# Performance work log

Measured on AMD Instinct MI355X. Metric: run time of the kernel, lower is better.

The kernel has to match this reference:

```python
import jax, jax.numpy as jnp
import numpy as np

B, S, T, M, H = 16, 128, 1024, 16, 1024
HID = 1024        # attention MLP hidden
WIDTH_EMB = 20    # width embedding dim
N_LING = 2        # len(linguistic_feature_types)


def setup_inputs() -> dict:
    key = jax.random.key(0)
    ks = jax.random.split(key, 12)
    doc_embeddings = jax.random.normal(ks[0], (B, T, H), dtype=jnp.float32)
    start_mappings = jax.random.normal(ks[1], (B, S, T), dtype=jnp.float32)
    end_mappings = jax.random.normal(ks[2], (B, S, T), dtype=jnp.float32)
    continuous_mappings = jax.random.normal(ks[3], (B, S, M, T), dtype=jnp.float32)
    width = jax.random.randint(ks[4], (B, S), 0, M, dtype=jnp.int64)
    linguistic_labels = jax.random.normal(ks[5], (B, S, N_LING), dtype=jnp.float32)
    # attention MLP params (torch Linear layout transposed to x @ W + b)
    W1 = jax.random.normal(ks[6], (H, HID), dtype=jnp.float32) * (1.0 / np.sqrt(H))
    b1 = jax.random.normal(ks[7], (HID,), dtype=jnp.float32) * 0.01
    W2 = jax.random.normal(ks[8], (HID, 1), dtype=jnp.float32) * (1.0 / np.sqrt(HID))
    b2 = jax.random.normal(ks[9], (1,), dtype=jnp.float32) * 0.01
    width_table = jax.random.normal(ks[10], (5, WIDTH_EMB), dtype=jnp.float32)
    return {
        'doc_embeddings': doc_embeddings,
        'start_mappings': start_mappings,
        'end_mappings': end_mappings,
        'continuous_mappings': continuous_mappings,
        'linguistic_labels': linguistic_labels,
        'W1': W1, 'b1': b1, 'W2': W2, 'b2': b2,
        'width_table': width_table,
        'width': width,
    }


def reference(doc_embeddings, start_mappings, end_mappings, continuous_mappings,
              linguistic_labels, W1, b1, W2, b2, width_table, width):
    # one-hot matmul gathers
    start = jnp.einsum('bst,bth->bsh', start_mappings, doc_embeddings)
    end = jnp.einsum('bst,bth->bsh', end_mappings, doc_embeddings)
    cont = jnp.einsum('bsmt,bth->bsmh', continuous_mappings, doc_embeddings)
    b, s, m, h = cont.shape
    vector = jnp.concatenate([start, end], axis=-1).reshape(b * s, 2 * h)
    cont = cont.reshape(b * s, m, h)
    w = width.reshape(b * s)
    ling = linguistic_labels.reshape(b * s, -1)
    # padded masked attention pooling
    masks = (jnp.arange(m)[None, :] < jnp.maximum(w, 1)[:, None]).astype(cont.dtype)
    hdn = jax.nn.relu(jnp.einsum('nmh,hk->nmk', cont, W1) + b1)
    scores = (jnp.einsum('nmk,ko->nmo', hdn, W2) + b2)[..., 0]  # [n, m]
    scores = scores * masks
    scores = jnp.where(scores != 0, scores, jnp.asarray(-9e9, scores.dtype))
    att = jax.nn.softmax(scores, axis=1)
    weighted_sum = jnp.einsum('nm,nmh->nh', att, cont)
    vector = jnp.concatenate([vector, weighted_sum], axis=1)
    # linguistic feature columns (loop over fixed small feature list)
    for fi in range(N_LING):
        vector = jnp.concatenate([vector, ling[:, fi:fi + 1]], axis=1)
    # width embedding (clamp max=4)
    wemb = width_table[jnp.clip(w, 0, 4)]
    vector = jnp.concatenate([vector, wemb], axis=1)
    return vector.reshape(b, s, -1)
```

## Files before the change

### kernel.cpp

```cpp
#include <hip/hip_runtime.h>

typedef unsigned short ushort_t;
typedef unsigned int uint_t;
typedef _Float16 f16;
typedef f16 f16x8 __attribute__((ext_vector_type(8)));
typedef float f32x4 __attribute__((ext_vector_type(4)));

#define B_   16
#define S_   128
#define T_   1024
#define M_   16
#define H_   1024
#define OUTW 3094
#define NSPAN (B_*S_)
#define NROW  (NSPAN*M_)

#define WS_CONT   0
#define WS_DOCT   67108864
#define WS_W1T    100663296
#define WS_SCORES 102760448
#define WS_A16    102891520
#define WS_NEED_A16 178388992ULL

__device__ __forceinline__ float sane(float v) {
  return fminf(fmaxf(v, -60000.f), 60000.f);
}
__device__ __forceinline__ ushort_t f16bits(float f) {
  union { f16 h; ushort_t u; } c; c.h = (f16)f; return c.u;
}
__device__ __forceinline__ void load_lds16(const void* g, void* l) {
  __builtin_amdgcn_global_load_lds(
      (const __attribute__((address_space(1))) uint_t*)g,
      (__attribute__((address_space(3))) uint_t*)l, 16, 0, 0);
}

__device__ __forceinline__ void tconv1024(const float* __restrict__ ip,
                                          ushort_t* __restrict__ op,
                                          uint_t (*tile)[65],
                                          int bx, int by, int tid) {
  const int c0 = bx * 64, r0 = by * 64;
  const int tx = tid & 63, ty = tid >> 6;
#pragma unroll
  for (int p = 0; p < 16; ++p) {
    int r = p * 4 + ty;
    tile[r][tx] = (uint_t)f16bits(ip[(size_t)(r0 + r) * 1024 + c0 + tx]);
  }
  __syncthreads();
  const int rr = (tid & 31) * 2, cc0 = tid >> 5;
  uint_t* op32 = (uint_t*)op;
#pragma unroll
  for (int p = 0; p < 8; ++p) {
    int c = cc0 + p * 8;
    uint_t lo = tile[rr][c] & 0xffffu;
    uint_t hi = tile[rr + 1][c] & 0xffffu;
    op32[((size_t)(c0 + c) * 1024 + r0 + rr) >> 1] = lo | (hi << 16);
  }
}

__global__ __launch_bounds__(256) void prep(const float* __restrict__ doc,
                                            ushort_t* __restrict__ docT,
                                            const float* __restrict__ W1,
                                            ushort_t* __restrict__ W1T,
                                            const float* __restrict__ startm,
                                            const float* __restrict__ endm,
                                            const float* __restrict__ contm,
                                            f16* __restrict__ A16,
                                            float* __restrict__ scores) {
  __shared__ uint_t tile[64][65];
  const int blk = blockIdx.x;
  const int tid = threadIdx.x;
  if (blk < 4096) {
    const int z = blk >> 8, by = (blk >> 4) & 15, bx = blk & 15;
    const size_t mo = (size_t)z * 1024 * 1024;
    tconv1024(doc + mo, docT + mo, tile, bx, by, tid);
  } else if (blk < 4352) {
    const int r2 = blk - 4096;
    tconv1024(W1, W1T, tile, r2 & 15, r2 >> 4, tid);
  } else if (blk < 6400) {
    const int lb = blk - 4352;
    uint_t c = (uint_t)lb * 256u + (uint_t)tid;
#pragma unroll 1
    for (int it = 0; it < 9; ++it) {
      const uint_t b   = c / 294912u;
      const uint_t rem = c - b * 294912u;
      const uint_t r   = rem >> 7;
      const uint_t col = (rem & 127u) << 3;
      const float* src;
      if (r < 128u)      src = startm + ((size_t)b * S_ + r) * T_;
      else if (r < 256u) src = endm + ((size_t)b * S_ + (r - 128u)) * T_;
      else               src = contm + ((size_t)b * S_ * M_ + (r - 256u)) * T_;
      f32x4 lo = *(const f32x4*)(src + col);
      f32x4 hi = *(const f32x4*)(src + col + 4);
      f16x8 h;
#pragma unroll
      for (int k = 0; k < 4; ++k) { h[k] = (f16)lo[k]; h[k + 4] = (f16)hi[k]; }
      *(f16x8*)(A16 + ((size_t)b * 2304 + r) * T_ + col) = h;
      c += 2048u * 256u;
    }
  } else {
    const int idx = (blk - 6400) * 256 + tid;
    scores[idx] = 0.f;
  }
}

__global__ __launch_bounds__(256) void tconv(const float* __restrict__ in,
                                             ushort_t* __restrict__ out,
                                             int R, int C) {
  __shared__ uint_t tile[64][65];
  const int tid = threadIdx.x;
  const size_t mo = (size_t)blockIdx.z * R * C;
  tconv1024(in + mo, out + mo, tile, blockIdx.x, blockIdx.y, tid);
}

__global__ __launch_bounds__(256) void gemm1f(const f16* __restrict__ A16,
                                              const ushort_t* __restrict__ docT,
                                              float* __restrict__ out,
                                              f16* __restrict__ contF) {
  __shared__ f16 As[128 * 32];
  __shared__ ushort_t Bs[128 * 32];
  const int tid = threadIdx.x;
  const uint_t pid = blockIdx.x;
  const int xcd = pid & 7;
  const int s_  = pid >> 3;
  const int ct  = s_ & 7;
  const int pg  = (s_ >> 3) * 8 + xcd;
  const int rt  = pg >> 4;
  const int b   = pg & 15;

  const f16* Ap = A16 + ((size_t)b * 2304 + (size_t)rt * 128) * T_;
  const ushort_t* Bp = docT + (size_t)b * (H_ * T_) + (size_t)ct * 128 * T_;

  const int lane = tid & 63, w = tid >> 6;
  const int wr = w >> 1, wc = w & 1;
  const int quad = lane >> 4, l16 = lane & 15;
  const int srow = lane >> 2;
  const int scol = ((lane & 3) ^ ((lane >> 3) & 3)) * 8;

  f32x4 acc[4][4];
#pragma unroll
  for (int i = 0; i < 4; ++i)
#pragma unroll
    for (int j = 0; j < 4; ++j) acc[i][j] = (f32x4){0.f, 0.f, 0.f, 0.f};

  for (int k0 = 0; k0 < T_; k0 += 32) {
#pragma unroll
    for (int i = 0; i < 2; ++i) {
      const int rb = w * 32 + i * 16;
      load_lds16(Ap + (size_t)(rb + srow) * T_ + k0 + scol, &As[rb * 32]);
    }
#pragma unroll
    for (int i = 0; i < 2; ++i) {
      const int rb = w * 32 + i * 16;
      load_lds16(Bp + (size_t)(rb + srow) * T_ + k0 + scol, &Bs[rb * 32]);
    }
    __syncthreads();
    f16x8 af[4], bfr[4];
#pragma unroll
    for (int i = 0; i < 4; ++i) {
      const int row = wr * 64 + i * 16 + l16;
      const int sw = (row >> 1) & 3;
      af[i] = *(const f16x8*)&As[row * 32 + ((quad ^ sw) * 8)];
    }
#pragma unroll
    for (int j = 0; j < 4; ++j) {
      const int row = wc * 64 + j * 16 + l16;
      const int sw = (row >> 1) & 3;
      bfr[j] = *(const f16x8*)&Bs[row * 32 + ((quad ^ sw) * 8)];
    }
#pragma unroll
    for (int i = 0; i < 4; ++i)
#pragma unroll
      for (int j = 0; j < 4; ++j)
        acc[i][j] = __builtin_amdgcn_mfma_f32_16x16x32_f16(af[i], bfr[j], acc[i][j], 0, 0, 0);
    __syncthreads();
  }

  if (rt < 2) {
    float* op = out + (size_t)b * S_ * OUTW + (size_t)rt * 1024 + (size_t)ct * 128;
#pragma unroll
    for (int i = 0; i < 4; ++i)
#pragma unroll
      for (int j = 0; j < 4; ++j)
#pragma unroll
        for (int r = 0; r < 4; ++r) {
          int row = wr * 64 + i * 16 + quad * 4 + r;
          int col = wc * 64 + j * 16 + l16;
          op[(size_t)row * OUTW + col] = sane(acc[i][j][r]);
        }
  } else {
    f16* cp = contF + ((size_t)b * 2048 + (size_t)(rt - 2) * 128) * H_ + (size_t)ct * 128;
#pragma unroll
    for (int i = 0; i < 4; ++i)
#pragma unroll
      for (int j = 0; j < 4; ++j)
#pragma unroll
        for (int r = 0; r < 4; ++r) {
          int row = wr * 64 + i * 16 + quad * 4 + r;
          int col = wc * 64 + j * 16 + l16;
          cp[(size_t)row * H_ + col] = (f16)sane(acc[i][j][r]);
        }
  }
}

__global__ __launch_bounds__(256) void gemm1(const float* __restrict__ startm,
                                             const float* __restrict__ endm,
                                             const float* __restrict__ contm,
                                             const ushort_t* __restrict__ docT,
                                             float* __restrict__ out,
                                             f16* __restrict__ contF) {
  __shared__ float As[128 * 32];
  __shared__ ushort_t Bs[128 * 32];
  const int tid = threadIdx.x;
  const uint_t pid = blockIdx.x;
  const int xcd = pid & 7;
  const int s_  = pid >> 3;
  const int ct  = s_ & 7;
  const int pg  = (s_ >> 3) * 8 + xcd;
  const int rt  = pg >> 4;
  const int b   = pg & 15;

  const float* Ap;
  if (rt == 0)      Ap = startm + (size_t)b * S_ * T_;
  else if (rt == 1) Ap = endm + (size_t)b * S_ * T_;
  else              Ap = contm + (size_t)b * (S_ * M_ * T_) + (size_t)(rt - 2) * 128 * T_;
  const ushort_t* Bp = docT + (size_t)b * (H_ * T_) + (size_t)ct * 128 * T_;

  const int lane = tid & 63, w = tid >> 6;
  const int wr = w >> 1, wc = w & 1;
  const int quad = lane >> 4, l16 = lane & 15;
  const int arow = lane >> 3;
  const int acol = ((lane & 7) ^ arow) * 4;
  const int brow = lane >> 2;
  const int bcol = ((lane & 3) ^ ((lane >> 3) & 3)) * 8;

  f32x4 acc[4][4];
#pragma unroll
  for (int i = 0; i < 4; ++i)
#pragma unroll
    for (int j = 0; j < 4; ++j) acc[i][j] = (f32x4){0.f, 0.f, 0.f, 0.f};

  for (int k0 = 0; k0 < T_; k0 += 32) {
#pragma unroll
    for (int i = 0; i < 4; ++i) {
      const int rb = w * 32 + i * 8;
      load_lds16(Ap + (size_t)(rb + arow) * T_ + k0 + acol, &As[rb * 32]);
    }
#pragma unroll
    for (int i = 0; i < 2; ++i) {
      const int rb = w * 32 + i * 16;
      load_lds16(Bp + (size_t)(rb + brow) * T_ + k0 + bcol, &Bs[rb * 32]);
    }
    __syncthreads();
    f16x8 af[4], bfr[4];
#pragma unroll
    for (int i = 0; i < 4; ++i) {
      const int row = wr * 64 + i * 16 + l16;
      const int sw = row & 7;
      f32x4 lo = *(const f32x4*)&As[row * 32 + (((quad * 2) ^ sw) * 4)];
      f32x4 hi = *(const f32x4*)&As[row * 32 + (((quad * 2 + 1) ^ sw) * 4)];
      f16x8 h;
#pragma unroll
      for (int k = 0; k < 4; ++k) { h[k] = (f16)lo[k]; h[k + 4] = (f16)hi[k]; }
      af[i] = h;
    }
#pragma unroll
    for (int j = 0; j < 4; ++j) {
      const int row = wc * 64 + j * 16 + l16;
      const int sw = (row >> 1) & 3;
      bfr[j] = *(const f16x8*)&Bs[row * 32 + ((quad ^ sw) * 8)];
    }
#pragma unroll
    for (int i = 0; i < 4; ++i)
#pragma unroll
      for (int j = 0; j < 4; ++j)
        acc[i][j] = __builtin_amdgcn_mfma_f32_16x16x32_f16(af[i], bfr[j], acc[i][j], 0, 0, 0);
    __syncthreads();
  }

  if (rt < 2) {
    float* op = out + (size_t)b * S_ * OUTW + (size_t)rt * 1024 + (size_t)ct * 128;
#pragma unroll
    for (int i = 0; i < 4; ++i)
#pragma unroll
      for (int j = 0; j < 4; ++j)
#pragma unroll
        for (int r = 0; r < 4; ++r) {
          int row = wr * 64 + i * 16 + quad * 4 + r;
          int col = wc * 64 + j * 16 + l16;
          op[(size_t)row * OUTW + col] = sane(acc[i][j][r]);
        }
  } else {
    f16* cp = contF + ((size_t)b * 2048 + (size_t)(rt - 2) * 128) * H_ + (size_t)ct * 128;
#pragma unroll
    for (int i = 0; i < 4; ++i)
#pragma unroll
      for (int j = 0; j < 4; ++j)
#pragma unroll
        for (int r = 0; r < 4; ++r) {
          int row = wr * 64 + i * 16 + quad * 4 + r;
          int col = wc * 64 + j * 16 + l16;
          cp[(size_t)row * H_ + col] = (f16)sane(acc[i][j][r]);
        }
  }
}

__global__ __launch_bounds__(512) void gemm2(const f16* __restrict__ contF,
                                             const f16* __restrict__ W1T,
                                             const float* __restrict__ b1,
                                             const float* __restrict__ W2,
                                             float* __restrict__ scores) {
  __shared__ f16 As[128 * 32];
  __shared__ f16 Bs[256 * 32];
  const int tid = threadIdx.x;
  const uint_t pid = blockIdx.x;
  const int xcd = pid & 7;
  const int s_  = pid >> 3;
  const int ct  = s_ & 3;
  const int g   = s_ >> 2;
  const int rt  = g * 8 + xcd;

  const f16* Ap = contF + (size_t)rt * 128 * H_;
  const f16* Bp = W1T + (size_t)ct * 256 * H_;

  const int lane = tid & 63, w = tid >> 6;
  const int wr = w >> 2;
  const int wc = w & 3;
  const int quad = lane >> 4, l16 = lane & 15;
  const int srow = lane >> 2;
  const int scol = ((lane & 3) ^ ((lane >> 3) & 3)) * 8;

  f32x4 acc[4][4];
#pragma unroll
  for (int i = 0; i < 4; ++i)
#pragma unroll
    for (int j = 0; j < 4; ++j) acc[i][j] = (f32x4){0.f, 0.f, 0.f, 0.f};

  for (int k0 = 0; k0 < H_; k0 += 32) {
    {
      const int rb = w * 16;
      load_lds16(Ap + (size_t)(rb + srow) * H_ + k0 + scol, &As[rb * 32]);
    }
#pragma unroll
    for (int i = 0; i < 2; ++i) {
      const int rb = i * 128 + w * 16;
      load_lds16(Bp + (size_t)(rb + srow) * H_ + k0 + scol, &Bs[rb * 32]);
    }
    __syncthreads();
    f16x8 af[4], bfr[4];
#pragma unroll
    for (int i = 0; i < 4; ++i) {
      const int row = wr * 64 + i * 16 + l16;
      const int sw = (row >> 1) & 3;
      af[i] = *(const f16x8*)&As[row * 32 + ((quad ^ sw) * 8)];
    }
#pragma unroll
    for (int j = 0; j < 4; ++j) {
      const int row = wc * 64 + j * 16 + l16;
      const int sw = (row >> 1) & 3;
      bfr[j] = *(const f16x8*)&Bs[row * 32 + ((quad ^ sw) * 8)];
    }
#pragma unroll
    for (int i = 0; i < 4; ++i)
#pragma unroll
      for (int j = 0; j < 4; ++j)
        acc[i][j] = __builtin_amdgcn_mfma_f32_16x16x32_f16(af[i], bfr[j], acc[i][j], 0, 0, 0);
    __syncthreads();
  }

  const int colbase = ct * 256 + wc * 64;
#pragma unroll
  for (int i = 0; i < 4; ++i) {
#pragma unroll
    for (int r = 0; r < 4; ++r) {
      float t = 0.f;
#pragma unroll
      for (int j = 0; j < 4; ++j) {
        int c = colbase + j * 16 + l16;
        float v = acc[i][j][r] + b1[c];
        v = fmaxf(v, 0.f);
        t = fmaf(v, W2[c], t);
      }
      t += __shfl_xor(t, 1);
      t += __shfl_xor(t, 2);
      t += __shfl_xor(t, 4);
      t += __shfl_xor(t, 8);
      if (l16 == 0) {
        int row = rt * 128 + wr * 64 + i * 16 + quad * 4 + r;
        atomicAdd(&scores[row], t);
      }
    }
  }
}

__global__ __launch_bounds__(256) void finalize(const f16* __restrict__ contF,
                                                const float* __restrict__ scores,
                                                const float* __restrict__ ling,
                                                const float* __restrict__ b2,
                                                const float* __restrict__ wtab,
                                                const int* __restrict__ width,
                                                float* __restrict__ out) {
  const int n = blockIdx.x;
  const int tid = threadIdx.x;
  __shared__ float sc[16];
  if (tid < 16) {
    float raw = scores[n * 16 + tid] + b2[0];
    if (raw != raw) raw = 0.0f;
    int wv = width[n];
    int wm = wv > 1 ? wv : 1;
    float s = (tid < wm) ? raw : 0.0f;
    if (s == 0.0f) s = -9e9f;
    sc[tid] = s;
  }
  __syncthreads();
  float mx = sc[0];
#pragma unroll
  for (int m = 1; m < 16; ++m) mx = fmaxf(mx, sc[m]);
  float e[16];
  float ssum = 0.f;
#pragma unroll
  for (int m = 0; m < 16; ++m) { e[m] = __expf(sc[m] - mx); ssum += e[m]; }
  const float inv = 1.0f / ssum;
  const f16* cp = contF + (size_t)n * (M_ * H_);
  float* op = out + (size_t)n * OUTW;
#pragma unroll
  for (int hh = 0; hh < 4; ++hh) {
    int h = tid + hh * 256;
    float a = 0.f;
#pragma unroll
    for (int m = 0; m < 16; ++m) a = fmaf(e[m], (float)cp[m * H_ + h], a);
    op[2048 + h] = sane(a * inv);
  }
  if (tid < 2) op[3072 + tid] = ling[n * 2 + tid];
  if (tid < 20) {
    int wv = width[n];
    int wcl = wv < 4 ? wv : 4;
    if (wcl < 0) wcl = 0;
    op[3074 + tid] = wtab[wcl * 20 + tid];
  }
}

extern "C" void kernel_launch(void* const* d_in, const int* in_sizes, int n_in,
                              void* d_out, int out_size, void* d_ws, size_t ws_size,
                              hipStream_t stream) {
  const float* doc    = (const float*)d_in[0];
  const float* startm = (const float*)d_in[1];
  const float* endm   = (const float*)d_in[2];
  const float* contm  = (const float*)d_in[3];
  const float* ling   = (const float*)d_in[4];
  const float* W1     = (const float*)d_in[5];
  const float* b1     = (const float*)d_in[6];
  const float* W2     = (const float*)d_in[7];
  const float* b2     = (const float*)d_in[8];
  const float* wtab   = (const float*)d_in[9];
  const int*   width  = (const int*)d_in[10];
  float* out = (float*)d_out;

  char* ws = (char*)d_ws;
  f16*      contF  = (f16*)(ws + WS_CONT);
  ushort_t* docT   = (ushort_t*)(ws + WS_DOCT);
  f16*      W1T    = (f16*)(ws + WS_W1T);
  float*    scores = (float*)(ws + WS_SCORES);
  f16*      A16    = (f16*)(ws + WS_A16);

  if (ws_size >= WS_NEED_A16) {
    prep<<<dim3(6528, 1, 1), 256, 0, stream>>>(doc, docT, W1, (ushort_t*)W1T,
                                               startm, endm, contm, A16, scores);
    gemm1f<<<dim3(2304, 1, 1), 256, 0, stream>>>(A16, docT, out, contF);
  } else {
    hipMemsetAsync(scores, 0, NROW * sizeof(float), stream);
    tconv<<<dim3(16, 16, 16), 256, 0, stream>>>(doc, docT, 1024, 1024);
    tconv<<<dim3(16, 16, 1), 256, 0, stream>>>(W1, (ushort_t*)W1T, 1024, 1024);
    gemm1<<<dim3(2304, 1, 1), 256, 0, stream>>>(startm, endm, contm, docT, out, contF);
  }
  gemm2<<<dim3(1024, 1, 1), 512, 0, stream>>>(contF, (const f16*)W1T, b1, W2, scores);
  finalize<<<dim3(NSPAN, 1, 1), 256, 0, stream>>>(contF, scores, ling, b2, wtab, width, out);
}
```

Baseline: 474.5 us.

## Widen gemm1f tile to 128x256 with 512 threads and vectorize loads

The first GEMM now uses 512-thread blocks covering 256 output columns instead of 128, which halves the block count and lets each A tile be reused across twice as many columns. The transpose/convert helper reads float4 vectors instead of scalars, and the finalize kernel reads four f16 values per load and accumulates four outputs per thread. The aim is less redundant A-tile traffic and fewer, wider memory transactions. The trade-off is more LDS per block and fewer blocks, which may lower occupancy or tail balance, and the finalize store pattern changes.

```diff
diff --git a/kernel.cpp b/kernel.cpp
--- a/kernel.cpp
+++ b/kernel.cpp
@@ -4,6 +4,7 @@
 typedef unsigned int uint_t;
 typedef _Float16 f16;
 typedef f16 f16x8 __attribute__((ext_vector_type(8)));
+typedef f16 f16x4 __attribute__((ext_vector_type(4)));
 typedef float f32x4 __attribute__((ext_vector_type(4)));
 
 #define B_   16
@@ -39,11 +40,14 @@
                                           uint_t (*tile)[65],
                                           int bx, int by, int tid) {
   const int c0 = bx * 64, r0 = by * 64;
-  const int tx = tid & 63, ty = tid >> 6;
-#pragma unroll
-  for (int p = 0; p < 16; ++p) {
-    int r = p * 4 + ty;
-    tile[r][tx] = (uint_t)f16bits(ip[(size_t)(r0 + r) * 1024 + c0 + tx]);
+  const int tx4 = (tid & 15) * 4;
+  const int ty4 = tid >> 4;
+#pragma unroll
+  for (int p = 0; p < 4; ++p) {
+    int r = p * 16 + ty4;
+    f32x4 v = *(const f32x4*)&ip[(size_t)(r0 + r) * 1024 + c0 + tx4];
+#pragma unroll
+    for (int k = 0; k < 4; ++k) tile[r][tx4 + k] = (uint_t)f16bits(v[k]);
   }
   __syncthreads();
   const int rr = (tid & 31) * 2, cc0 = tid >> 5;
@@ -112,26 +116,27 @@
   tconv1024(in + mo, out + mo, tile, blockIdx.x, blockIdx.y, tid);
 }
 
-__global__ __launch_bounds__(256) void gemm1f(const f16* __restrict__ A16,
+__global__ __launch_bounds__(512) void gemm1f(const f16* __restrict__ A16,
                                               const ushort_t* __restrict__ docT,
                                               float* __restrict__ out,
                                               f16* __restrict__ contF) {
   __shared__ f16 As[128 * 32];
-  __shared__ ushort_t Bs[128 * 32];
+  __shared__ ushort_t Bs[256 * 32];
   const int tid = threadIdx.x;
   const uint_t pid = blockIdx.x;
   const int xcd = pid & 7;
   const int s_  = pid >> 3;
-  const int ct  = s_ & 7;
-  const int pg  = (s_ >> 3) * 8 + xcd;
+  const int ct  = s_ & 3;
+  const int pg  = (s_ >> 2) * 8 + xcd;
   const int rt  = pg >> 4;
   const int b   = pg & 15;
 
   const f16* Ap = A16 + ((size_t)b * 2304 + (size_t)rt * 128) * T_;
-  const ushort_t* Bp = docT + (size_t)b * (H_ * T_) + (size_t)ct * 128 * T_;
+  const ushort_t* Bp = docT + (size_t)b * (H_ * T_) + (size_t)ct * 256 * T_;
 
   const int lane = tid & 63, w = tid >> 6;
-  const int wr = w >> 1, wc = w & 1;
+  const int wr = w >> 2;
+  const int wc = w & 3;
   const int quad = lane >> 4, l16 = lane & 15;
   const int srow = lane >> 2;
   const int scol = ((lane & 3) ^ ((lane >> 3) & 3)) * 8;
@@ -143,14 +148,13 @@
     for (int j = 0; j < 4; ++j) acc[i][j] = (f32x4){0.f, 0.f, 0.f, 0.f};
 
   for (int k0 = 0; k0 < T_; k0 += 32) {
+    {
+      const int rb = w * 16;
+      load_lds16(Ap + (size_t)(rb + srow) * T_ + k0 + scol, &As[rb * 32]);
+    }
 #pragma unroll
     for (int i = 0; i < 2; ++i) {
-      const int rb = w * 32 + i * 16;
-      load_lds16(Ap + (size_t)(rb + srow) * T_ + k0 + scol, &As[rb * 32]);
-    }
-#pragma unroll
-    for (int i = 0; i < 2; ++i) {
-      const int rb = w * 32 + i * 16;
+      const int rb = i * 128 + w * 16;
       load_lds16(Bp + (size_t)(rb + srow) * T_ + k0 + scol, &Bs[rb * 32]);
     }
     __syncthreads();
@@ -176,7 +180,7 @@
   }
 
   if (rt < 2) {
-    float* op = out + (size_t)b * S_ * OUTW + (size_t)rt * 1024 + (size_t)ct * 128;
+    float* op = out + (size_t)b * S_ * OUTW + (size_t)rt * 1024 + (size_t)ct * 256;
 #pragma unroll
     for (int i = 0; i < 4; ++i)
 #pragma unroll
@@ -188,7 +192,7 @@
           op[(size_t)row * OUTW + col] = sane(acc[i][j][r]);
         }
   } else {
-    f16* cp = contF + ((size_t)b * 2048 + (size_t)(rt - 2) * 128) * H_ + (size_t)ct * 128;
+    f16* cp = contF + ((size_t)b * 2048 + (size_t)(rt - 2) * 128) * H_ + (size_t)ct * 256;
 #pragma unroll
     for (int i = 0; i < 4; ++i)
 #pragma unroll
@@ -422,14 +426,20 @@
   const float inv = 1.0f / ssum;
   const f16* cp = contF + (size_t)n * (M_ * H_);
   float* op = out + (size_t)n * OUTW;
-#pragma unroll
-  for (int hh = 0; hh < 4; ++hh) {
-    int h = tid + hh * 256;
-    float a = 0.f;
-#pragma unroll
-    for (int m = 0; m < 16; ++m) a = fmaf(e[m], (float)cp[m * H_ + h], a);
-    op[2048 + h] = sane(a * inv);
-  }
+  const int h0 = tid * 4;
+  float a0 = 0.f, a1 = 0.f, a2 = 0.f, a3 = 0.f;
+#pragma unroll
+  for (int m = 0; m < 16; ++m) {
+    f16x4 v = *(const f16x4*)&cp[m * H_ + h0];
+    a0 = fmaf(e[m], (float)v[0], a0);
+    a1 = fmaf(e[m], (float)v[1], a1);
+    a2 = fmaf(e[m], (float)v[2], a2);
+    a3 = fmaf(e[m], (float)v[3], a3);
+  }
+  op[2048 + h0 + 0] = sane(a0 * inv);
+  op[2048 + h0 + 1] = sane(a1 * inv);
+  op[2048 + h0 + 2] = sane(a2 * inv);
+  op[2048 + h0 + 3] = sane(a3 * inv);
   if (tid < 2) op[3072 + tid] = ling[n * 2 + tid];
   if (tid < 20) {
     int wv = width[n];
@@ -465,7 +475,7 @@
   if (ws_size >= WS_NEED_A16) {
     prep<<<dim3(6528, 1, 1), 256, 0, stream>>>(doc, docT, W1, (ushort_t*)W1T,
                                                startm, endm, contm, A16, scores);
-    gemm1f<<<dim3(2304, 1, 1), 256, 0, stream>>>(A16, docT, out, contF);
+    gemm1f<<<dim3(1152, 1, 1), 512, 0, stream>>>(A16, docT, out, contF);
   } else {
     hipMemsetAsync(scores, 0, NROW * sizeof(float), stream);
     tconv<<<dim3(16, 16, 16), 256, 0, stream>>>(doc, docT, 1024, 1024);
```

Result: slower. 488.8 us (+3.0%).
